# Kernel optimization log

Measured on AMD Instinct MI355X. Metric: run time of the kernel, lower is better.

Reference implementation:

```python
import jax, jax.numpy as jnp
import numpy as np

EMBED_SIZE = 1024

def setup_inputs() -> dict:
    key = jax.random.key(0)
    k1, k2, k3, k4 = jax.random.split(key, 4)
    B, T, C, H = 8, 2048, 1024, 128
    embeddings = jax.random.normal(k1, (B, T, C), dtype=jnp.float32)
    # nn.Linear(embed, head, bias=False) weight applied as x @ W^T; store as [C, H] for x @ W
    scale = 1.0 / np.sqrt(C)
    Wq = jax.random.normal(k2, (C, H), dtype=jnp.float32) * scale
    Wk = jax.random.normal(k3, (C, H), dtype=jnp.float32) * scale
    Wv = jax.random.normal(k4, (C, H), dtype=jnp.float32) * scale
    return {"embeddings": embeddings, "Wq": Wq, "Wk": Wk, "Wv": Wv}

def reference(embeddings, Wq, Wk, Wv):
    B, T, C = embeddings.shape
    q = jnp.einsum('btc,ch->bth', embeddings, Wq)
    k = jnp.einsum('btc,ch->bth', embeddings, Wk)
    v = jnp.einsum('btc,ch->bth', embeddings, Wv)
    # NOTE: source scales by embed_size**-0.5 (not head_size**-0.5)
    wei = jnp.einsum('bqh,bkh->bqk', q, k) * (C ** -0.5)
    causal = jnp.tril(jnp.ones((T, T), dtype=bool))  # tril buffer
    wei = jnp.where(causal, wei, -jnp.inf)
    wei = jax.nn.softmax(wei, axis=-1)
    return jnp.einsum('bqk,bkh->bqh', wei, v)
```

## Files before the change

### kernel.cpp

```cpp
#include <hip/hip_runtime.h>
#include <hip/hip_bf16.h>

typedef __bf16 bf16x8 __attribute__((ext_vector_type(8)));
typedef float f32x4 __attribute__((ext_vector_type(4)));
typedef ushort us8 __attribute__((ext_vector_type(8)));

#define MFMA(a, b, c) __builtin_amdgcn_mfma_f32_16x16x32_bf16((a), (b), (c), 0, 0, 0)

static constexpr int T_LEN = 2048;
static constexpr int C_DIM = 1024;
static constexpr int H_DIM = 128;
static constexpr int M_ROWS = 8 * 2048;
static constexpr int N_COLS = 384;
static constexpr int SLOTS_PER_B = 528;
static constexpr int PSTR = 72;
static constexpr int KSTR = 136;
static constexpr int VSTR = 72;
static constexpr int BSTR = 40;

__device__ __forceinline__ ushort f2bf(float f) {
  union { float f; unsigned u; } v; v.f = f;
  unsigned u = v.u;
  u += 0x7fffu + ((u >> 16) & 1u);
  return (ushort)(u >> 16);
}
__device__ __forceinline__ float bf2f(ushort u) {
  union { unsigned u; float f; } v; v.u = (unsigned)u << 16;
  return v.f;
}

__global__ void wt_convert(const float* __restrict__ Wq,
                           const float* __restrict__ Wk,
                           const float* __restrict__ Wv,
                           ushort* __restrict__ wt) {
  int o = blockIdx.x * 256 + threadIdx.x;
  int kt = o / 12288;
  int rem = o - kt * 12288;
  int gc = rem >> 5;
  int kk = rem & 31;
  int c  = kt * 32 + kk;
  int mat = gc >> 7;
  int h   = gc & 127;
  const float* W = (mat == 0) ? Wq : ((mat == 1) ? Wk : Wv);
  wt[o] = f2bf(W[c * H_DIM + h]);
}

__global__ __launch_bounds__(256, 4) void qkv_gemm(const float* __restrict__ X,
                                                   const ushort* __restrict__ wt,
                                                   ushort* __restrict__ qws,
                                                   ushort* __restrict__ kws,
                                                   ushort* __restrict__ vtws) {
  __shared__ ushort As[2][32 * BSTR];
  __shared__ ushort Bs[2][192 * BSTR];
  const int tid = threadIdx.x;
  const int wid = tid >> 6, lane = tid & 63;
  const int lg = lane >> 4, lr = lane & 15;
  const int m0 = (blockIdx.x >> 1) * 32;
  const int n0 = (blockIdx.x & 1) * 192;
  const float QSCL = 0.03125f * 1.44269504f;

  const int ar = tid >> 3, ac = tid & 7;
  const float* gA = &X[(size_t)(m0 + ar) * C_DIM + ac * 4];

  const int u0 = tid * 24;
  const int br0 = u0 >> 5,        bk0 = u0 & 31;
  const int br1 = (u0 + 8) >> 5,  bk1 = (u0 + 8) & 31;
  const int br2 = (u0 + 16) >> 5, bk2 = (u0 + 16) & 31;

  f32x4 acc[2][3];
#pragma unroll
  for (int r = 0; r < 2; ++r)
#pragma unroll
    for (int c = 0; c < 3; ++c)
      acc[r][c] = f32x4{0.f, 0.f, 0.f, 0.f};

  float4 areg = *(const float4*)gA;
  const ushort* gB0 = &wt[(size_t)(0 * 384 + n0) * 32 + u0];
  us8 breg0 = *(const us8*)(gB0);
  us8 breg1 = *(const us8*)(gB0 + 8);
  us8 breg2 = *(const us8*)(gB0 + 16);

  for (int kt = 0; kt < 32; ++kt) {
    const int cur = kt & 1;
    __syncthreads();
    {
      ushort4 av;
      av.x = f2bf(areg.x); av.y = f2bf(areg.y);
      av.z = f2bf(areg.z); av.w = f2bf(areg.w);
      *(ushort4*)&As[cur][ar * BSTR + ac * 4] = av;
      *(us8*)&Bs[cur][br0 * BSTR + bk0] = breg0;
      *(us8*)&Bs[cur][br1 * BSTR + bk1] = breg1;
      *(us8*)&Bs[cur][br2 * BSTR + bk2] = breg2;
    }
    if (kt + 1 < 32) {
      areg = *(const float4*)(gA + (kt + 1) * 32);
      const ushort* gB = &wt[(size_t)((kt + 1) * 384 + n0) * 32 + u0];
      breg0 = *(const us8*)(gB);
      breg1 = *(const us8*)(gB + 8);
      breg2 = *(const us8*)(gB + 16);
    }
    __syncthreads();

    bf16x8 a0 = *(const bf16x8*)&As[cur][(lr) * BSTR + lg * 8];
    bf16x8 a1 = *(const bf16x8*)&As[cur][(16 + lr) * BSTR + lg * 8];
#pragma unroll
    for (int c = 0; c < 3; ++c) {
      bf16x8 bf = *(const bf16x8*)&Bs[cur][(wid * 48 + c * 16 + lr) * BSTR + lg * 8];
      acc[0][c] = MFMA(a0, bf, acc[0][c]);
      acc[1][c] = MFMA(a1, bf, acc[1][c]);
    }
  }

#pragma unroll
  for (int c = 0; c < 3; ++c) {
    int gc = n0 + wid * 48 + c * 16 + lr;
    int mat = gc >> 7, h = gc & 127;
#pragma unroll
    for (int r = 0; r < 2; ++r) {
#pragma unroll
      for (int j = 0; j < 4; ++j) {
        int gr = m0 + r * 16 + lg * 4 + j;
        float val = acc[r][c][j];
        ushort ov = f2bf(mat == 0 ? val * QSCL : val);
        if (mat == 0) {
          qws[(size_t)gr * H_DIM + h] = ov;
        } else if (mat == 1) {
          kws[(size_t)gr * H_DIM + h] = ov;
        } else {
          int b = gr >> 11, t = gr & 2047;
          vtws[((size_t)b * H_DIM + h) * T_LEN + t] = ov;
        }
      }
    }
  }
}

__global__ __launch_bounds__(256, 3) void attn_part(const ushort* __restrict__ qws,
                                                    const ushort* __restrict__ kws,
                                                    const ushort* __restrict__ vtws,
                                                    float* __restrict__ pml,
                                                    ushort* __restrict__ pacc,
                                                    float* __restrict__ out) {
  __shared__ ushort Klds[64 * KSTR];
  __shared__ ushort Vlds[128 * VSTR];
  __shared__ ushort Pw[4][16 * PSTR];

  const int tid = threadIdx.x;
  const int wid = tid >> 6, lane = tid & 63;
  const int lg = lane >> 4, lr = lane & 15;
  const int bid = blockIdx.x;
  const int b = bid & 7;
  const int item = bid >> 3;

  int qb, ck;
  bool direct;
  if (item < 8) {
    qb = item; ck = 0; direct = true;
  } else {
    const int p = item - 8;
    direct = false;
    if (p < 12)      { int q = p / 3;        qb = 8 + q;  ck = p - q * 3; }
    else if (p < 28) { int q = (p - 12) >> 2; qb = 12 + q; ck = (p - 12) & 3; }
    else if (p < 48) { int q = (p - 28) / 5; qb = 16 + q; ck = (p - 28) - q * 5; }
    else if (p < 72) { int q = (p - 48) / 6; qb = 20 + q; ck = (p - 48) - q * 6; }
    else if (p < 100){ int q = (p - 72) / 7; qb = 24 + q; ck = (p - 72) - q * 7; }
    else             { int q = (p - 100) >> 3; qb = 28 + q; ck = (p - 100) & 7; }
  }
  const int qi = qb * 4 + wid;
  const int q0 = qi * 16;
  const int nt = qb + 1;
  const int kvt_lo = direct ? 0 : ck * 4;
  const int kvt_hi = direct ? nt : min(ck * 4 + 4, nt);
  const size_t tokbase = (size_t)b * T_LEN;
  const ushort* vb = vtws + (size_t)b * H_DIM * T_LEN;

  const int kr = tid >> 2, kseg = tid & 3;
  const int vr = tid >> 1, vseg = tid & 1;
  const ushort* gK = &kws[(tokbase + kr) * H_DIM + kseg * 32];
  const ushort* gV = &vb[(size_t)vr * T_LEN + vseg * 32];

  bf16x8 qf[4];
#pragma unroll
  for (int hk = 0; hk < 4; ++hk)
    qf[hk] = *(const bf16x8*)&qws[(tokbase + q0 + lr) * H_DIM + hk * 32 + lg * 8];

  f32x4 acc[8];
#pragma unroll
  for (int hf = 0; hf < 8; ++hf) acc[hf] = f32x4{0.f, 0.f, 0.f, 0.f};
  float mrun = -INFINITY, lrun = 0.f;

  ushort* Pme = &Pw[wid][0];

  us8 kreg[4], vreg[4];
#pragma unroll
  for (int i = 0; i < 4; ++i) {
    kreg[i] = *(const us8*)(gK + (size_t)kvt_lo * 64 * H_DIM + i * 8);
    vreg[i] = *(const us8*)(gV + kvt_lo * 64 + i * 8);
  }

  for (int kvt = kvt_lo; kvt < kvt_hi; ++kvt) {
    const int kv0 = kvt * 64;

    __syncthreads();
#pragma unroll
    for (int i = 0; i < 4; ++i) {
      *(us8*)&Klds[kr * KSTR + kseg * 32 + i * 8] = kreg[i];
      *(us8*)&Vlds[vr * VSTR + vseg * 32 + i * 8] = vreg[i];
    }
    if (kvt + 1 < kvt_hi) {
#pragma unroll
      for (int i = 0; i < 4; ++i) {
        kreg[i] = *(const us8*)(gK + (size_t)(kv0 + 64) * H_DIM + i * 8);
        vreg[i] = *(const us8*)(gV + kv0 + 64 + i * 8);
      }
    }
    __syncthreads();

    f32x4 s[4];
#pragma unroll
    for (int c = 0; c < 4; ++c) {
      f32x4 sc = f32x4{0.f, 0.f, 0.f, 0.f};
#pragma unroll
      for (int hk = 0; hk < 4; ++hk) {
        bf16x8 kf = *(const bf16x8*)&Klds[(c * 16 + lr) * KSTR + hk * 32 + lg * 8];
        sc = MFMA(kf, qf[hk], sc);
      }
      s[c] = sc;
    }

    if (kvt == nt - 1) {
#pragma unroll
      for (int c = 0; c < 4; ++c)
#pragma unroll
        for (int j = 0; j < 4; ++j) {
          int kv = kv0 + c * 16 + lg * 4 + j;
          if (kv > q0 + lr) s[c][j] = -INFINITY;
        }
    }

    float mx = s[0][0];
#pragma unroll
    for (int c = 0; c < 4; ++c)
#pragma unroll
      for (int j = 0; j < 4; ++j) mx = fmaxf(mx, s[c][j]);
    mx = fmaxf(mx, __shfl_xor(mx, 16));
    mx = fmaxf(mx, __shfl_xor(mx, 32));

    float mnew = fmaxf(mrun, mx);
    float scold = exp2f(mrun - mnew);

    float rsum = 0.f;
#pragma unroll
    for (int c = 0; c < 4; ++c)
#pragma unroll
      for (int j = 0; j < 4; ++j) {
        float p = exp2f(s[c][j] - mnew);
        s[c][j] = p;
        rsum += p;
      }

#pragma unroll
    for (int c = 0; c < 4; ++c) {
      ushort4 u;
      u.x = f2bf(s[c][0]); u.y = f2bf(s[c][1]);
      u.z = f2bf(s[c][2]); u.w = f2bf(s[c][3]);
      *(ushort4*)&Pme[lr * PSTR + c * 16 + lg * 4] = u;
    }

    bf16x8 v0[8];
#pragma unroll
    for (int hf = 0; hf < 8; ++hf)
      v0[hf] = *(const bf16x8*)&Vlds[(hf * 16 + lr) * VSTR + lg * 8];

    rsum += __shfl_xor(rsum, 16);
    rsum += __shfl_xor(rsum, 32);

    lrun = lrun * scold + rsum;
    mrun = mnew;
#pragma unroll
    for (int hf = 0; hf < 8; ++hf)
#pragma unroll
      for (int j = 0; j < 4; ++j) acc[hf][j] *= scold;

    bf16x8 pa0 = *(const bf16x8*)&Pme[lr * PSTR + lg * 8];
    bf16x8 pa1 = *(const bf16x8*)&Pme[lr * PSTR + 32 + lg * 8];

#pragma unroll
    for (int hf = 0; hf < 8; ++hf)
      acc[hf] = MFMA(v0[hf], pa0, acc[hf]);
#pragma unroll
    for (int hf = 0; hf < 8; ++hf) {
      bf16x8 v1 = *(const bf16x8*)&Vlds[(hf * 16 + lr) * VSTR + 32 + lg * 8];
      acc[hf] = MFMA(v1, pa1, acc[hf]);
    }
  }

  if (direct) {
    float inv = 1.0f / lrun;
    float* op = &out[(tokbase + q0 + lr) * H_DIM + lg * 4];
#pragma unroll
    for (int hf = 0; hf < 8; ++hf) {
      float4 r0 = make_float4(acc[hf][0] * inv, acc[hf][1] * inv,
                              acc[hf][2] * inv, acc[hf][3] * inv);
      *(float4*)(op + hf * 16) = r0;
    }
  } else {
    int base;
    if (qi < 48)       base = (qi - 32) * 3;
    else if (qi < 64)  base = 48 + (qi - 48) * 4;
    else if (qi < 80)  base = 112 + (qi - 64) * 5;
    else if (qi < 96)  base = 192 + (qi - 80) * 6;
    else if (qi < 112) base = 288 + (qi - 96) * 7;
    else               base = 400 + (qi - 112) * 8;
    const size_t slot = (size_t)b * SLOTS_PER_B + base + ck;
    if (lg == 0) {
      pml[slot * 32 + lr] = mrun;
      pml[slot * 32 + 16 + lr] = lrun;
    }
    ushort* ap = &pacc[slot * 2048 + (size_t)lr * 128 + lg * 4];
#pragma unroll
    for (int hf = 0; hf < 8; ++hf) {
      ushort4 u;
      u.x = f2bf(acc[hf][0]); u.y = f2bf(acc[hf][1]);
      u.z = f2bf(acc[hf][2]); u.w = f2bf(acc[hf][3]);
      *(ushort4*)(ap + hf * 16) = u;
    }
  }
}

__global__ __launch_bounds__(256) void attn_merge(const float* __restrict__ pml,
                                                  const ushort* __restrict__ pacc,
                                                  float* __restrict__ out) {
  const int bid = blockIdx.x;
  const int b = bid & 7, qi = (bid >> 3) + 32;
  int base, nch;
  if (qi < 48)       { base = (qi - 32) * 3;        nch = 3; }
  else if (qi < 64)  { base = 48 + (qi - 48) * 4;   nch = 4; }
  else if (qi < 80)  { base = 112 + (qi - 64) * 5;  nch = 5; }
  else if (qi < 96)  { base = 192 + (qi - 80) * 6;  nch = 6; }
  else if (qi < 112) { base = 288 + (qi - 96) * 7;  nch = 7; }
  else               { base = 400 + (qi - 112) * 8; nch = 8; }
  const size_t slot0 = (size_t)b * SLOTS_PER_B + base;
  const int tid = threadIdx.x;
  const int r = tid >> 4, c0 = (tid & 15) * 8;

  float mrun = -INFINITY, L = 0.f;
  float o[8];
#pragma unroll
  for (int i = 0; i < 8; ++i) o[i] = 0.f;

  for (int ck = 0; ck < nch; ++ck) {
    const size_t s = slot0 + ck;
    float m = pml[s * 32 + r];
    float l = pml[s * 32 + 16 + r];
    float mn = fmaxf(mrun, m);
    float sc = exp2f(mrun - mn);
    float w  = exp2f(m - mn);
    L = L * sc + w * l;
    const ushort* ap = &pacc[s * 2048 + (size_t)r * 128 + c0];
    ushort4 u0 = *(const ushort4*)ap;
    ushort4 u1 = *(const ushort4*)(ap + 4);
    o[0] = o[0] * sc + w * bf2f(u0.x); o[1] = o[1] * sc + w * bf2f(u0.y);
    o[2] = o[2] * sc + w * bf2f(u0.z); o[3] = o[3] * sc + w * bf2f(u0.w);
    o[4] = o[4] * sc + w * bf2f(u1.x); o[5] = o[5] * sc + w * bf2f(u1.y);
    o[6] = o[6] * sc + w * bf2f(u1.z); o[7] = o[7] * sc + w * bf2f(u1.w);
    mrun = mn;
  }
  float invL = 1.0f / L;
  float4 r0 = make_float4(o[0] * invL, o[1] * invL, o[2] * invL, o[3] * invL);
  float4 r1 = make_float4(o[4] * invL, o[5] * invL, o[6] * invL, o[7] * invL);
  float* op = &out[((size_t)b * T_LEN + qi * 16 + r) * H_DIM + c0];
  *(float4*)op = r0;
  *(float4*)(op + 4) = r1;
}

extern "C" void kernel_launch(void* const* d_in, const int* in_sizes, int n_in,
                              void* d_out, int out_size, void* d_ws, size_t ws_size,
                              hipStream_t stream) {
  const float* emb = (const float*)d_in[0];
  const float* Wq  = (const float*)d_in[1];
  const float* Wk  = (const float*)d_in[2];
  const float* Wv  = (const float*)d_in[3];
  float* out = (float*)d_out;

  ushort* wt   = (ushort*)d_ws;
  ushort* qws  = wt  + (size_t)N_COLS * C_DIM;
  ushort* kws  = qws + (size_t)M_ROWS * H_DIM;
  ushort* vtws = kws + (size_t)M_ROWS * H_DIM;
  ushort* pacc = vtws + (size_t)8 * H_DIM * T_LEN;
  float*  pml  = (float*)d_ws;

  wt_convert<<<(N_COLS * C_DIM) / 256, 256, 0, stream>>>(Wq, Wk, Wv, wt);
  qkv_gemm<<<(M_ROWS / 32) * 2, 256, 0, stream>>>(emb, wt, qws, kws, vtws);
  attn_part<<<8 * 140, 256, 0, stream>>>(qws, kws, vtws, pml, pacc, out);
  attn_merge<<<8 * 96, 256, 0, stream>>>(pml, pacc, out);
}
```

Measured before the change: 80.80 us.

## Swizzle QKV GEMM shared tiles and deepen prefetch to two stages

New measurement: 78.62 us. 1.03x faster.

```diff
diff --git a/kernel.cpp b/kernel.cpp
--- a/kernel.cpp
+++ b/kernel.cpp
@@ -16,7 +16,6 @@
 static constexpr int PSTR = 72;
 static constexpr int KSTR = 136;
 static constexpr int VSTR = 72;
-static constexpr int BSTR = 40;
 
 __device__ __forceinline__ ushort f2bf(float f) {
   union { float f; unsigned u; } v; v.f = f;
@@ -27,6 +26,16 @@
 __device__ __forceinline__ float bf2f(ushort u) {
   union { unsigned u; float f; } v; v.u = (unsigned)u << 16;
   return v.f;
+}
+
+__device__ __forceinline__ void waitbar() {
+  asm volatile("s_waitcnt lgkmcnt(0)" ::: "memory");
+  __builtin_amdgcn_s_barrier();
+  __builtin_amdgcn_sched_barrier(0);
+}
+
+__device__ __forceinline__ int swz_byte(int row, int slot) {
+  return (row >> 1) * 128 + (row & 1) * 64 + ((slot * 16) ^ (((row >> 1) & 3) << 4));
 }
 
 __global__ void wt_convert(const float* __restrict__ Wq,
@@ -50,8 +59,8 @@
                                                    ushort* __restrict__ qws,
                                                    ushort* __restrict__ kws,
                                                    ushort* __restrict__ vtws) {
-  __shared__ ushort As[2][32 * BSTR];
-  __shared__ ushort Bs[2][192 * BSTR];
+  __shared__ ushort As[2][16 * 64];
+  __shared__ ushort Bs[2][96 * 64];
   const int tid = threadIdx.x;
   const int wid = tid >> 6, lane = tid & 63;
   const int lg = lane >> 4, lr = lane & 15;
@@ -59,13 +68,15 @@
   const int n0 = (blockIdx.x & 1) * 192;
   const float QSCL = 0.03125f * 1.44269504f;
 
-  const int ar = tid >> 3, ac = tid & 7;
-  const float* gA = &X[(size_t)(m0 + ar) * C_DIM + ac * 4];
-
-  const int u0 = tid * 24;
-  const int br0 = u0 >> 5,        bk0 = u0 & 31;
-  const int br1 = (u0 + 8) >> 5,  bk1 = (u0 + 8) & 31;
-  const int br2 = (u0 + 16) >> 5, bk2 = (u0 + 16) & 31;
+  const int arow = tid >> 3, acol = tid & 7;
+  const float* gA = &X[(size_t)(m0 + arow) * C_DIM + acol * 4];
+  const int awb = swz_byte(arow, acol >> 1) + (acol & 1) * 8;
+
+  const ushort* gBt = wt + (size_t)n0 * 32 + (size_t)tid * 8;
+  const int bwb0 = swz_byte(tid >> 2, tid & 3);
+
+  const int afb = swz_byte(lr, lg);
+  const int bfb = swz_byte(wid * 48 + lr, lg);
 
   f32x4 acc[2][3];
 #pragma unroll
@@ -74,42 +85,65 @@
     for (int c = 0; c < 3; ++c)
       acc[r][c] = f32x4{0.f, 0.f, 0.f, 0.f};
 
-  float4 areg = *(const float4*)gA;
-  const ushort* gB0 = &wt[(size_t)(0 * 384 + n0) * 32 + u0];
-  us8 breg0 = *(const us8*)(gB0);
-  us8 breg1 = *(const us8*)(gB0 + 8);
-  us8 breg2 = *(const us8*)(gB0 + 16);
-
-  for (int kt = 0; kt < 32; ++kt) {
-    const int cur = kt & 1;
-    __syncthreads();
-    {
-      ushort4 av;
-      av.x = f2bf(areg.x); av.y = f2bf(areg.y);
-      av.z = f2bf(areg.z); av.w = f2bf(areg.w);
-      *(ushort4*)&As[cur][ar * BSTR + ac * 4] = av;
-      *(us8*)&Bs[cur][br0 * BSTR + bk0] = breg0;
-      *(us8*)&Bs[cur][br1 * BSTR + bk1] = breg1;
-      *(us8*)&Bs[cur][br2 * BSTR + bk2] = breg2;
-    }
-    if (kt + 1 < 32) {
-      areg = *(const float4*)(gA + (kt + 1) * 32);
-      const ushort* gB = &wt[(size_t)((kt + 1) * 384 + n0) * 32 + u0];
-      breg0 = *(const us8*)(gB);
-      breg1 = *(const us8*)(gB + 8);
-      breg2 = *(const us8*)(gB + 16);
-    }
-    __syncthreads();
-
-    bf16x8 a0 = *(const bf16x8*)&As[cur][(lr) * BSTR + lg * 8];
-    bf16x8 a1 = *(const bf16x8*)&As[cur][(16 + lr) * BSTR + lg * 8];
-#pragma unroll
-    for (int c = 0; c < 3; ++c) {
-      bf16x8 bf = *(const bf16x8*)&Bs[cur][(wid * 48 + c * 16 + lr) * BSTR + lg * 8];
-      acc[0][c] = MFMA(a0, bf, acc[0][c]);
-      acc[1][c] = MFMA(a1, bf, acc[1][c]);
-    }
-  }
+  float4 aE, aO;
+  us8 bE0, bE1, bE2, bO0, bO1, bO2;
+
+#define LOAD_A(dst, kt_) dst = *(const float4*)(gA + (kt_) * 32);
+#define LOAD_B(b0, b1, b2, kt_)                                   \
+  {                                                               \
+    const ushort* g_ = gBt + (size_t)(kt_) * 12288;               \
+    b0 = *(const us8*)(g_);                                       \
+    b1 = *(const us8*)(g_ + 2048);                                \
+    b2 = *(const us8*)(g_ + 4096);                                \
+  }
+#define WRITE_SET(aS, b0, b1, b2, buf)                            \
+  {                                                               \
+    ushort4 av;                                                   \
+    av.x = f2bf(aS.x); av.y = f2bf(aS.y);                         \
+    av.z = f2bf(aS.z); av.w = f2bf(aS.w);                         \
+    *(ushort4*)((char*)&As[buf][0] + awb) = av;                   \
+    *(us8*)((char*)&Bs[buf][0] + bwb0) = b0;                      \
+    *(us8*)((char*)&Bs[buf][0] + bwb0 + 4096) = b1;               \
+    *(us8*)((char*)&Bs[buf][0] + bwb0 + 8192) = b2;               \
+  }
+#define COMPUTE(buf)                                              \
+  {                                                               \
+    bf16x8 a0 = *(const bf16x8*)((const char*)&As[buf][0] + afb); \
+    bf16x8 a1 = *(const bf16x8*)((const char*)&As[buf][0] + afb + 1024); \
+    _Pragma("unroll")                                             \
+    for (int c = 0; c < 3; ++c) {                                 \
+      bf16x8 bf = *(const bf16x8*)((const char*)&Bs[buf][0] + bfb + c * 1024); \
+      acc[0][c] = MFMA(a0, bf, acc[0][c]);                        \
+      acc[1][c] = MFMA(a1, bf, acc[1][c]);                        \
+    }                                                             \
+  }
+
+  {
+    float4 aT;
+    us8 bT0, bT1, bT2;
+    LOAD_A(aT, 0);
+    LOAD_B(bT0, bT1, bT2, 0);
+    WRITE_SET(aT, bT0, bT1, bT2, 0);
+  }
+  LOAD_A(aE, 1); LOAD_B(bE0, bE1, bE2, 1);
+  LOAD_A(aO, 2); LOAD_B(bO0, bO1, bO2, 2);
+  waitbar();
+
+  for (int k2 = 0; k2 < 32; k2 += 2) {
+    WRITE_SET(aE, bE0, bE1, bE2, 1);
+    if (k2 + 3 < 32) { LOAD_A(aE, k2 + 3); LOAD_B(bE0, bE1, bE2, k2 + 3); }
+    COMPUTE(0);
+    waitbar();
+
+    if (k2 + 2 < 32) WRITE_SET(aO, bO0, bO1, bO2, 0);
+    if (k2 + 4 < 32) { LOAD_A(aO, k2 + 4); LOAD_B(bO0, bO1, bO2, k2 + 4); }
+    COMPUTE(1);
+    waitbar();
+  }
+#undef LOAD_A
+#undef LOAD_B
+#undef WRITE_SET
+#undef COMPUTE
 
 #pragma unroll
   for (int c = 0; c < 3; ++c) {
```
